# Optimization experiments

Hardware: AMD Instinct MI355X
Metric: run time of the kernel (lower is better)

## Reference

```python
import jax, jax.numpy as jnp
import numpy as np

TOP_K = 256  # int(channels[0])


def setup_inputs() -> dict:
    key = jax.random.key(0)
    x = jax.random.normal(key, (1, 1024, 256, 256), dtype=jnp.float32)
    return {"x": x}


def reference(x):
    # Per-channel mean over the squeezed [C, H, W] tensor (batch==1), then
    # 'strong' mode: sort descending by mean and take top TOP_K channel indices.
    means = jnp.mean(x[0], axis=(1, 2))  # [C]
    _, idx = jax.lax.top_k(means, TOP_K)  # descending means -> strongest channels
    return idx
```

## Files before the change

kernel.cpp:

```cpp
#include <hip/hip_runtime.h>
#include <stdint.h>

#define NCH   1024
#define HW    65536
#define TOPK  256

__global__ __launch_bounds__(256) void channel_mean_kernel(
    const float* __restrict__ x, float* __restrict__ means) {
    const int c   = blockIdx.x;
    const int tid = threadIdx.x;
    const float4* p = (const float4*)(x + (size_t)c * HW);

    double acc = 0.0;
    #pragma unroll 4
    for (int i = tid; i < HW / 4; i += 256) {
        float4 v = p[i];
        acc += (double)v.x + (double)v.y + (double)v.z + (double)v.w;
    }

    #pragma unroll
    for (int off = 32; off > 0; off >>= 1)
        acc += __shfl_down(acc, off, 64);

    __shared__ double lds[4];
    const int wave = tid >> 6;
    const int lane = tid & 63;
    if (lane == 0) lds[wave] = acc;
    __syncthreads();
    if (tid == 0) {
        double s = lds[0] + lds[1] + lds[2] + lds[3];
        means[c] = (float)(s / (double)HW);
    }
}

__global__ __launch_bounds__(1024) void topk_kernel(
    const float* __restrict__ means, int* __restrict__ out) {
    __shared__ unsigned long long keys[NCH];
    const int tid = threadIdx.x;

    float f = means[tid];
    unsigned int u = __float_as_uint(f);
    u = (u & 0x80000000u) ? ~u : (u | 0x80000000u);
    keys[tid] = ((unsigned long long)u << 32) |
                (unsigned long long)(0xFFFFFFFFu - (unsigned)tid);
    __syncthreads();

    for (int k = 2; k <= NCH; k <<= 1) {
        for (int j = k >> 1; j > 0; j >>= 1) {
            const int ixj = tid ^ j;
            if (ixj > tid) {
                unsigned long long a = keys[tid];
                unsigned long long b = keys[ixj];
                const bool descending = ((tid & k) == 0);
                if ((a < b) == descending) {
                    keys[tid] = b;
                    keys[ixj] = a;
                }
            }
            __syncthreads();
        }
    }

    if (tid < TOPK) {
        out[tid] = (int)(0xFFFFFFFFu - (unsigned)(keys[tid] & 0xFFFFFFFFull));
    }
}

extern "C" void kernel_launch(void* const* d_in, const int* in_sizes, int n_in,
                              void* d_out, int out_size, void* d_ws, size_t ws_size,
                              hipStream_t stream) {
    const float* x   = (const float*)d_in[0];
    float* means     = (float*)d_ws;
    int*   out       = (int*)d_out;

    channel_mean_kernel<<<NCH, 256, 0, stream>>>(x, means);
    topk_kernel<<<1, 1024, 0, stream>>>(means, out);
}
```

Before: 362.5 us.

## Split channel reduction across four blocks and sort top-k with wave shuffles

The channel-mean reduction now launches four blocks per channel. Each block fully unrolls 16 float4 loads with four independent double accumulators and writes a partial sum. The top-k kernel combines the partials and runs the bitonic sort in registers, using wave-level shuffles for strides under 64 and shared memory only for larger strides, which cuts barriers and LDS traffic. The cost is a larger workspace for the double partials and a few extra global reads in the sort kernel.

```diff
diff --git a/kernel.cpp b/kernel.cpp
--- a/kernel.cpp
+++ b/kernel.cpp
@@ -1,78 +1,108 @@
 #include <hip/hip_runtime.h>
 #include <stdint.h>
 
-#define NCH   1024
-#define HW    65536
-#define TOPK  256
+#define NCH    1024
+#define HW     65536
+#define TOPK   256
+#define PARTS  4
+#define BLK    256
 
-__global__ __launch_bounds__(256) void channel_mean_kernel(
-    const float* __restrict__ x, float* __restrict__ means) {
-    const int c   = blockIdx.x;
-    const int tid = threadIdx.x;
-    const float4* p = (const float4*)(x + (size_t)c * HW);
+__global__ __launch_bounds__(BLK) void channel_partial_kernel(
+    const float* __restrict__ x, double* __restrict__ partials) {
+    const int b    = blockIdx.x;
+    const int c    = b >> 2;
+    const int part = b & 3;
+    const int tid  = threadIdx.x;
 
-    double acc = 0.0;
-    #pragma unroll 4
-    for (int i = tid; i < HW / 4; i += 256) {
-        float4 v = p[i];
-        acc += (double)v.x + (double)v.y + (double)v.z + (double)v.w;
+    const float4* p = (const float4*)(x + ((size_t)c << 16) + ((size_t)part << 14));
+
+    double a0 = 0.0, a1 = 0.0, a2 = 0.0, a3 = 0.0;
+    #pragma unroll
+    for (int t = 0; t < 16; t += 4) {
+        float4 v0 = p[tid + (t + 0) * BLK];
+        float4 v1 = p[tid + (t + 1) * BLK];
+        float4 v2 = p[tid + (t + 2) * BLK];
+        float4 v3 = p[tid + (t + 3) * BLK];
+        a0 += (double)v0.x + (double)v0.y + (double)v0.z + (double)v0.w;
+        a1 += (double)v1.x + (double)v1.y + (double)v1.z + (double)v1.w;
+        a2 += (double)v2.x + (double)v2.y + (double)v2.z + (double)v2.w;
+        a3 += (double)v3.x + (double)v3.y + (double)v3.z + (double)v3.w;
     }
+    double acc = (a0 + a1) + (a2 + a3);
 
     #pragma unroll
     for (int off = 32; off > 0; off >>= 1)
         acc += __shfl_down(acc, off, 64);
 
-    __shared__ double lds[4];
+    __shared__ double lds[BLK / 64];
     const int wave = tid >> 6;
     const int lane = tid & 63;
     if (lane == 0) lds[wave] = acc;
     __syncthreads();
     if (tid == 0) {
-        double s = lds[0] + lds[1] + lds[2] + lds[3];
-        means[c] = (float)(s / (double)HW);
+        double s = ((lds[0] + lds[1]) + lds[2]) + lds[3];
+        partials[b] = s;
     }
 }
 
+__device__ __forceinline__ unsigned long long bitonic_step(
+    unsigned long long key, unsigned long long partner, int tid, int k, int j) {
+    const bool keep_max = (((tid & k) == 0) == ((tid & j) == 0));
+    if (keep_max) return (key > partner) ? key : partner;
+    return (key < partner) ? key : partner;
+}
+
 __global__ __launch_bounds__(1024) void topk_kernel(
-    const float* __restrict__ means, int* __restrict__ out) {
+    const double* __restrict__ partials, int* __restrict__ out) {
     __shared__ unsigned long long keys[NCH];
     const int tid = threadIdx.x;
 
-    float f = means[tid];
+    const double* p = partials + (size_t)tid * PARTS;
+    double s = ((p[0] + p[1]) + p[2]) + p[3];
+    float f = (float)(s * (1.0 / (double)HW));
+
     unsigned int u = __float_as_uint(f);
     u = (u & 0x80000000u) ? ~u : (u | 0x80000000u);
-    keys[tid] = ((unsigned long long)u << 32) |
-                (unsigned long long)(0xFFFFFFFFu - (unsigned)tid);
-    __syncthreads();
+    unsigned long long key = ((unsigned long long)u << 32) |
+                             (unsigned long long)(0xFFFFFFFFu - (unsigned)tid);
 
-    for (int k = 2; k <= NCH; k <<= 1) {
+    #pragma unroll
+    for (int k = 2; k <= 64; k <<= 1) {
+        #pragma unroll
         for (int j = k >> 1; j > 0; j >>= 1) {
-            const int ixj = tid ^ j;
-            if (ixj > tid) {
-                unsigned long long a = keys[tid];
-                unsigned long long b = keys[ixj];
-                const bool descending = ((tid & k) == 0);
-                if ((a < b) == descending) {
-                    keys[tid] = b;
-                    keys[ixj] = a;
-                }
-            }
+            unsigned long long partner = __shfl_xor(key, j, 64);
+            key = bitonic_step(key, partner, tid, k, j);
+        }
+    }
+
+    #pragma unroll
+    for (int k = 128; k <= 1024; k <<= 1) {
+        for (int j = k >> 1; j >= 64; j >>= 1) {
             __syncthreads();
+            keys[tid] = key;
+            __syncthreads();
+            unsigned long long partner = keys[tid ^ j];
+            key = bitonic_step(key, partner, tid, k, j);
+        }
+        #pragma unroll
+        for (int j = 32; j > 0; j >>= 1) {
+            unsigned long long partner = __shfl_xor(key, j, 64);
+            key = bitonic_step(key, partner, tid, k, j);
         }
     }
 
     if (tid < TOPK) {
-        out[tid] = (int)(0xFFFFFFFFu - (unsigned)(keys[tid] & 0xFFFFFFFFull));
+        out[tid] = (int)(0xFFFFFFFFu - (unsigned)(key & 0xFFFFFFFFull));
     }
 }
 
 extern "C" void kernel_launch(void* const* d_in, const int* in_sizes, int n_in,
                               void* d_out, int out_size, void* d_ws, size_t ws_size,
                               hipStream_t stream) {
-    const float* x   = (const float*)d_in[0];
-    float* means     = (float*)d_ws;
-    int*   out       = (int*)d_out;
+    const float* x     = (const float*)d_in[0];
+    double* partials   = (double*)d_ws;
+    int*    out        = (int*)d_out;
 
-    channel_mean_kernel<<<NCH, 256, 0, stream>>>(x, means);
-    topk_kernel<<<1, 1024, 0, stream>>>(means, out);
+    channel_partial_kernel<<<NCH * PARTS, BLK, 0, stream>>>(x, partials);
+    topk_kernel<<<1, NCH, 0, stream>>>(partials, out);
 }
```

Result: no change. 355.8 us (-1.8%).
